# Optimization experiments

Hardware: AMD Instinct MI355X
Metric: run time of the kernel (lower is better)

Reference implementation:

```python
import jax, jax.numpy as jnp
import numpy as np

ENERGY_PERCENT = 0.8


def setup_inputs() -> dict:
    key = jax.random.key(0)
    B, T, C = 32, 4096, 128
    x = jax.random.normal(key, (B, T, C), dtype=jnp.float32)
    return {"x": x}


def reference(x):
    # x: [B, T, C]; FFT along time axis.
    T = x.shape[1]
    xf = jnp.fft.rfft(x, axis=1)                      # [B, F, C] complex
    energies = jnp.abs(xf) ** 2                       # [B, F, C]

    # Sort energies descending along freq axis (per batch, per channel).
    sorted_indices = jnp.argsort(-energies, axis=1)   # [B, F, C] int
    sorted_energies = jnp.take_along_axis(energies, sorted_indices, axis=1)

    total_energy = jnp.sum(energies, axis=1, keepdims=True)        # [B, 1, C]
    cumulative = jnp.cumsum(sorted_energies, axis=1)               # [B, F, C]

    # Smallest k such that cumulative energy exceeds energy_percent of total.
    exceeded = cumulative > total_energy * ENERGY_PERCENT          # [B, F, C] bool
    k = jnp.argmax(exceeded, axis=1) + 1                           # [B, C]

    # rank[b, f, c] = position of frequency f in the descending energy order;
    # this is the inverse permutation of sorted_indices (argsort of a permutation).
    rank = jnp.argsort(sorted_indices, axis=1)                     # [B, F, C]

    is_low_freq = rank < k[:, None, :]                             # [B, F, C]

    # Zero out the high-energy ("low-frequency") components -> residual x_var.
    mask = jnp.where(is_low_freq, 0.0, 1.0).astype(x.dtype)        # [B, F, C]
    x_var = jnp.fft.irfft(xf * mask, n=T, axis=1)                  # [B, T, C]
    x_inv = x - x_var
    return (x_var, x_inv)
```

## Files before the change

### kernel.cpp

```cpp
#include <hip/hip_runtime.h>


#define TLEN 4096
#define N2   2048
#define CCH  128
#define BB   32
#define NSER (BB * CCH)
#define HALF 16777216
#define PI_F 3.14159265358979323846f
#define NT   64
#define TS   64
#define SLAB (CCH * TS)

#define LP(i) ((i) + ((i) >> 5))

__device__ __forceinline__ void cmul(float& r, float& i, float br, float bi) {
  float tr = r * br - i * bi;
  i = r * bi + i * br;
  r = tr;
}

__device__ __forceinline__ void dft4(float vr[4], float vi[4], float s) {
  float t0r = vr[0] + vr[2], t0i = vi[0] + vi[2];
  float t1r = vr[0] - vr[2], t1i = vi[0] - vi[2];
  float t2r = vr[1] + vr[3], t2i = vi[1] + vi[3];
  float d3r = vr[1] - vr[3], d3i = vi[1] - vi[3];
  float t3r = -s * d3i, t3i = s * d3r;
  vr[0] = t0r + t2r; vi[0] = t0i + t2i;
  vr[1] = t1r + t3r; vi[1] = t1i + t3i;
  vr[2] = t0r - t2r; vi[2] = t0i - t2i;
  vr[3] = t1r - t3r; vi[3] = t1i - t3i;
}

__device__ __forceinline__ void dft8(float vr[8], float vi[8], float s) {
  float er[4]  = {vr[0], vr[2], vr[4], vr[6]};
  float ei[4]  = {vi[0], vi[2], vi[4], vi[6]};
  float odr[4] = {vr[1], vr[3], vr[5], vr[7]};
  float odi[4] = {vi[1], vi[3], vi[5], vi[7]};
  dft4(er, ei, s);
  dft4(odr, odi, s);
  const float c = 0.70710678118654752440f;
  float wr[4] = {1.0f, c, 0.0f, -c};
  float wi[4] = {0.0f, s * c, s, s * c};
  #pragma unroll
  for (int k = 0; k < 4; ++k) {
    float tr = wr[k] * odr[k] - wi[k] * odi[k];
    float ti = wr[k] * odi[k] + wi[k] * odr[k];
    vr[k]     = er[k] + tr; vi[k]     = ei[k] + ti;
    vr[k + 4] = er[k] - tr; vi[k + 4] = ei[k] - ti;
  }
}

__device__ __forceinline__ void stage8_first(float* zr, float* zi, int tid, float s) {
  float vr[8], vi[8];
  #pragma unroll
  for (int r = 0; r < 8; ++r) {
    int idx = LP(tid + (r << 8));
    vr[r] = zr[idx]; vi[r] = zi[idx];
  }
  dft8(vr, vi, s);
  __syncthreads();
  #pragma unroll
  for (int r = 0; r < 8; ++r) {
    int idx = LP((tid << 3) + r);
    zr[idx] = vr[r]; zi[idx] = vi[r];
  }
  __syncthreads();
}

template <int NS>
__device__ __forceinline__ void stage8_tw(float* zr, float* zi, int tid, float s) {
  int j = tid;
  int p = j & (NS - 1);
  float vr[8], vi[8];
  #pragma unroll
  for (int r = 0; r < 8; ++r) {
    int idx = LP(j + (r << 8));
    vr[r] = zr[idx]; vi[r] = zi[idx];
  }
  float ang = s * 6.28318530717958647692f * (float)p / (float)(NS * 8);
  float s1, c1; __sincosf(ang, &s1, &c1);
  float c2 = c1 * c1 - s1 * s1, s2 = 2.0f * c1 * s1;
  float c3 = c2 * c1 - s2 * s1, s3 = c2 * s1 + s2 * c1;
  float c4 = c2 * c2 - s2 * s2, s4 = 2.0f * c2 * s2;
  float c5 = c4 * c1 - s4 * s1, s5 = c4 * s1 + s4 * c1;
  float c6 = c4 * c2 - s4 * s2, s6 = c4 * s2 + s4 * c2;
  float c7 = c4 * c3 - s4 * s3, s7 = c4 * s3 + s4 * c3;
  cmul(vr[1], vi[1], c1, s1);
  cmul(vr[2], vi[2], c2, s2);
  cmul(vr[3], vi[3], c3, s3);
  cmul(vr[4], vi[4], c4, s4);
  cmul(vr[5], vi[5], c5, s5);
  cmul(vr[6], vi[6], c6, s6);
  cmul(vr[7], vi[7], c7, s7);
  dft8(vr, vi, s);
  __syncthreads();
  int idxD = ((j - p) << 3) + p;
  #pragma unroll
  for (int r = 0; r < 8; ++r) {
    int idx = LP(idxD + r * NS);
    zr[idx] = vr[r]; zi[idx] = vi[r];
  }
  __syncthreads();
}

__device__ __forceinline__ void stage4_last(float* zr, float* zi, int tid, float s) {
  #pragma unroll
  for (int half = 0; half < 2; ++half) {
    int j = tid + (half << 8);
    float ang = s * PI_F * (float)j * (1.0f / 1024.0f);
    float s1, c1; __sincosf(ang, &s1, &c1);
    float c2 = c1 * c1 - s1 * s1, s2 = 2.0f * c1 * s1;
    float c3 = c2 * c1 - s2 * s1, s3 = c2 * s1 + s2 * c1;
    float vr[4], vi[4];
    #pragma unroll
    for (int r = 0; r < 4; ++r) {
      int idx = LP(j + (r << 9));
      vr[r] = zr[idx]; vi[r] = zi[idx];
    }
    cmul(vr[1], vi[1], c1, s1);
    cmul(vr[2], vi[2], c2, s2);
    cmul(vr[3], vi[3], c3, s3);
    dft4(vr, vi, s);
    #pragma unroll
    for (int r = 0; r < 4; ++r) {
      int idx = LP(j + (r << 9));
      zr[idx] = vr[r]; zi[idx] = vi[r];
    }
  }
  __syncthreads();
}

__device__ __forceinline__ void fft2048(float* zr, float* zi, int tid, float s) {
  stage8_first(zr, zi, tid, s);
  stage8_tw<8>(zr, zi, tid, s);
  stage8_tw<64>(zr, zi, tid, s);
  stage4_last(zr, zi, tid, s);
}

__device__ __forceinline__ float block_sum(float v, float* red, int tid, int bank) {
  #pragma unroll
  for (int o = 32; o > 0; o >>= 1) v += __shfl_down(v, o, 64);
  if ((tid & 63) == 0) red[(bank << 2) + (tid >> 6)] = v;
  __syncthreads();
  int b4 = bank << 2;
  return red[b4] + red[b4 + 1] + red[b4 + 2] + red[b4 + 3];
}

__global__ __launch_bounds__(256) void fourier_filter_series(float* __restrict__ buf) {
  __shared__ float zr[2113], zi[2113];
  __shared__ float red[8];
  int tid = threadIdx.x;
  int b = blockIdx.x >> 7, c = blockIdx.x & 127;
  float* bufp = buf + (size_t)b * (NT * SLAB) + (size_t)c * TS;

  #pragma unroll
  for (int j = 0; j < 8; ++j) {
    int k = tid + (j << 8);
    int off = ((k >> 5) << 13) + ((k & 31) << 1);
    float2 v = *(const float2*)(bufp + off);
    zr[LP(k)] = v.x; zi[LP(k)] = v.y;
  }
  __syncthreads();

  fft2048(zr, zi, tid, -1.0f);

  float eb[9];
  eb[8] = 0.0f;
  const float RC  = 0.92387953251128675613f;
  const float RSn = -0.38268343236508977173f;
  float ws, wc;
  __sincosf(-PI_F * (float)tid * (1.0f / 2048.0f), &ws, &wc);
  #pragma unroll
  for (int jj = 0; jj < 4; ++jj) {
    int k = tid + (jj << 8);
    int mkz = (N2 - k) & (N2 - 1);
    int ik = LP(k), im = LP(N2 - k);
    float akr = zr[ik],      aki = zi[ik];
    float bkr = zr[LP(mkz)], bki = zi[LP(mkz)];
    float Er  = 0.5f * (akr + bkr);
    float Ei  = 0.5f * (aki - bki);
    float Or_ = 0.5f * (aki + bki);
    float Oi  = 0.5f * (bkr - akr);
    float tr = wc * Or_ - ws * Oi;
    float ti = wc * Oi + ws * Or_;
    float x0r = Er + tr, x0i = Ei + ti;
    float x1r = Er - tr, x1i = ti - Ei;
    zr[ik] = x0r; zi[ik] = x0i;
    zr[im] = x1r; zi[im] = x1i;
    eb[2 * jj]     = x0r * x0r + x0i * x0i;
    eb[2 * jj + 1] = x1r * x1r + x1i * x1i;
    float nwc = wc * RC - ws * RSn;
    ws = wc * RSn + ws * RC; wc = nwc;
  }
  if (tid == 0) {
    int i4 = LP(1024);
    float re = zr[i4], im_ = zi[i4];
    zi[i4] = -im_;
    eb[8] = re * re + im_ * im_;
  }

  float tloc = 0.0f;
  #pragma unroll
  for (int s = 0; s < 9; ++s) tloc += eb[s];
  float total = block_sum(tloc, red, tid, 0);
  float thresh = 0.8f * total;

  unsigned lo = 0u, hi = 0x7F7FFFFFu;
  for (int it = 0; it < 31; ++it) {
    unsigned mid = (lo + hi + 1u) >> 1;
    float tau = __uint_as_float(mid);
    float loc = 0.0f;
    #pragma unroll
    for (int s = 0; s < 9; ++s) loc += (eb[s] >= tau) ? eb[s] : 0.0f;
    float ssum = block_sum(loc, red, tid, (it + 1) & 1);
    if (ssum > thresh) lo = mid; else hi = mid - 1;
  }
  float tau = __uint_as_float(lo);

  const float RSp = 0.38268343236508977173f;
  __sincosf(PI_F * (float)tid * (1.0f / 2048.0f), &ws, &wc);
  #pragma unroll
  for (int jj = 0; jj < 4; ++jj) {
    int k = tid + (jj << 8);
    int ik = LP(k), im = LP(N2 - k);
    float xkr = zr[ik], xki = zi[ik];
    float xmr = zr[im], xmi = zi[im];
    float ekk = xkr * xkr + xki * xki;
    float emm = xmr * xmr + xmi * xmi;
    if (ekk >= tau) { xkr = 0.0f; xki = 0.0f; }
    if (emm >= tau) { xmr = 0.0f; xmi = 0.0f; }
    float Er = 0.5f * (xkr + xmr);
    float Ei = 0.5f * (xki - xmi);
    float Br = 0.5f * (xkr - xmr);
    float Bi = 0.5f * (xki + xmi);
    float Or_ = wc * Br - ws * Bi;
    float Oi  = wc * Bi + ws * Br;
    zr[ik] = Er - Oi;  zi[ik] = Ei + Or_;
    zr[im] = Er + Oi;  zi[im] = Or_ - Ei;
    float nwc = wc * RC - ws * RSp;
    ws = wc * RSp + ws * RC; wc = nwc;
  }
  if (tid == 0) {
    int i4 = LP(1024);
    float re = zr[i4], im_ = zi[i4];
    float e = re * re + im_ * im_;
    if (e >= tau) { re = 0.0f; im_ = 0.0f; }
    zr[i4] = re; zi[i4] = -im_;
  }
  __syncthreads();

  fft2048(zr, zi, tid, 1.0f);

  const float scale = 1.0f / 2048.0f;
  #pragma unroll
  for (int j = 0; j < 8; ++j) {
    int k = tid + (j << 8);
    int off = ((k >> 5) << 13) + ((k & 31) << 1);
    float2 v;
    v.x = zr[LP(k)] * scale;
    v.y = zi[LP(k)] * scale;
    *(float2*)(bufp + off) = v;
  }
}

__global__ __launch_bounds__(512) void transpose_fwd(const float* __restrict__ x, float* __restrict__ buf) {
  __shared__ float lds[CCH * 65];
  int tb = blockIdx.x, b = blockIdx.y;
  const float* xp = x + ((size_t)b * TLEN + (size_t)tb * TS) * CCH;
  #pragma unroll
  for (int it = 0; it < 4; ++it) {
    int idx = threadIdx.x + (it << 9);
    int r = idx >> 5, c4 = (idx & 31) << 2;
    float4 v = *(const float4*)(xp + (size_t)r * CCH + c4);
    lds[(c4 + 0) * 65 + r] = v.x;
    lds[(c4 + 1) * 65 + r] = v.y;
    lds[(c4 + 2) * 65 + r] = v.z;
    lds[(c4 + 3) * 65 + r] = v.w;
  }
  __syncthreads();
  float* op = buf + ((size_t)b * NT + tb) * SLAB;
  #pragma unroll
  for (int it = 0; it < 4; ++it) {
    int idx = threadIdx.x + (it << 9);
    int c = idx >> 4, s4 = (idx & 15) << 2;
    float4 v;
    v.x = lds[c * 65 + s4 + 0];
    v.y = lds[c * 65 + s4 + 1];
    v.z = lds[c * 65 + s4 + 2];
    v.w = lds[c * 65 + s4 + 3];
    *(float4*)(op + c * TS + s4) = v;
  }
}

__global__ __launch_bounds__(512) void finalize_t(const float* __restrict__ buf, const float* __restrict__ x,
                                                  float* __restrict__ xvar, float* __restrict__ xinv) {
  __shared__ float lds[TS * 132];
  int tb = blockIdx.x, b = blockIdx.y;
  const float* ip = buf + ((size_t)b * NT + tb) * SLAB;
  #pragma unroll
  for (int it = 0; it < 4; ++it) {
    int idx = threadIdx.x + (it << 9);
    int c = idx >> 4, s4 = (idx & 15) << 2;
    float4 v = *(const float4*)(ip + c * TS + s4);
    lds[(s4 + 0) * 132 + c] = v.x;
    lds[(s4 + 1) * 132 + c] = v.y;
    lds[(s4 + 2) * 132 + c] = v.z;
    lds[(s4 + 3) * 132 + c] = v.w;
  }
  __syncthreads();
  size_t rowbase = ((size_t)b * TLEN + (size_t)tb * TS) * CCH;
  #pragma unroll
  for (int it = 0; it < 4; ++it) {
    int idx = threadIdx.x + (it << 9);
    int t = idx >> 5, c4 = (idx & 31) << 2;
    float4 v = *(const float4*)(&lds[t * 132 + c4]);
    size_t off = rowbase + (size_t)t * CCH + c4;
    float4 xv = *(const float4*)(x + off);
    *(float4*)(xvar + off) = v;
    *(float4*)(xinv + off) = make_float4(xv.x - v.x, xv.y - v.y, xv.z - v.z, xv.w - v.w);
  }
}

extern "C" void kernel_launch(void* const* d_in, const int* in_sizes, int n_in,
                              void* d_out, int out_size, void* d_ws, size_t ws_size,
                              hipStream_t stream) {
  const float* x = (const float*)d_in[0];
  float* out  = (float*)d_out;
  float* xvar = out;
  float* xinv = out + HALF;

  bool use_ws = ws_size >= (size_t)HALF * sizeof(float);
  float* buf = use_ws ? (float*)d_ws : xinv;

  dim3 tgrid(NT, BB);
  transpose_fwd<<<tgrid, 512, 0, stream>>>(x, buf);
  fourier_filter_series<<<NSER, 256, 0, stream>>>(buf);
  finalize_t<<<tgrid, 512, 0, stream>>>(buf, x, xvar, xinv);
}
```

Before: 301.2 us.

## Fuse forward transpose into FFT kernel with strided channel loads and LDS swizzle

The separate transpose_fwd kernel is removed. The FFT kernel now reads each channel's time series straight from x using strided scalar loads, with a block-to-channel remap meant to spread accesses across channels. The launch bound gains a minimum-occupancy hint, and finalize_t XOR-swizzles its LDS indices to cut bank conflicts. This drops one full read and write pass over the buffer and one kernel launch. The cost is uncoalesced 4-byte loads at a 1 KB stride, which depend on L2 reuse across neighbouring channel blocks.

```diff
diff --git a/kernel.cpp b/kernel.cpp
--- a/kernel.cpp
+++ b/kernel.cpp
@@ -147,19 +147,36 @@
   return red[b4] + red[b4 + 1] + red[b4 + 2] + red[b4 + 3];
 }
 
-__global__ __launch_bounds__(256) void fourier_filter_series(float* __restrict__ buf) {
+__global__ __launch_bounds__(256, 8) void fourier_filter_series(const float* __restrict__ x,
+                                                                float* __restrict__ buf) {
   __shared__ float zr[2113], zi[2113];
   __shared__ float red[8];
   int tid = threadIdx.x;
-  int b = blockIdx.x >> 7, c = blockIdx.x & 127;
-  float* bufp = buf + (size_t)b * (NT * SLAB) + (size_t)c * TS;
-
-  #pragma unroll
-  for (int j = 0; j < 8; ++j) {
-    int k = tid + (j << 8);
-    int off = ((k >> 5) << 13) + ((k & 31) << 1);
-    float2 v = *(const float2*)(bufp + off);
-    zr[LP(k)] = v.x; zi[LP(k)] = v.y;
+
+  int bid = blockIdx.x;
+  int r = bid & 7;
+  int m = bid >> 3;
+  int b = m >> 4;
+  int u = m & 15;
+  int c = (((r + b) & 7) << 4) | u;
+
+  const float* xp = x + ((size_t)b * TLEN) * CCH + c;
+  #pragma unroll
+  for (int jb = 0; jb < 2; ++jb) {
+    float re[4], im[4];
+    #pragma unroll
+    for (int j = 0; j < 4; ++j) {
+      int k = tid + (((jb << 2) + j) << 8);
+      int off = k << 8;
+      re[j] = xp[off];
+      im[j] = xp[off + CCH];
+    }
+    #pragma unroll
+    for (int j = 0; j < 4; ++j) {
+      int k = tid + (((jb << 2) + j) << 8);
+      zr[LP(k)] = re[j];
+      zi[LP(k)] = im[j];
+    }
   }
   __syncthreads();
 
@@ -252,6 +269,7 @@
 
   fft2048(zr, zi, tid, 1.0f);
 
+  float* bufp = buf + (size_t)b * (NT * SLAB) + (size_t)c * TS;
   const float scale = 1.0f / 2048.0f;
   #pragma unroll
   for (int j = 0; j < 8; ++j) {
@@ -264,35 +282,6 @@
   }
 }
 
-__global__ __launch_bounds__(512) void transpose_fwd(const float* __restrict__ x, float* __restrict__ buf) {
-  __shared__ float lds[CCH * 65];
-  int tb = blockIdx.x, b = blockIdx.y;
-  const float* xp = x + ((size_t)b * TLEN + (size_t)tb * TS) * CCH;
-  #pragma unroll
-  for (int it = 0; it < 4; ++it) {
-    int idx = threadIdx.x + (it << 9);
-    int r = idx >> 5, c4 = (idx & 31) << 2;
-    float4 v = *(const float4*)(xp + (size_t)r * CCH + c4);
-    lds[(c4 + 0) * 65 + r] = v.x;
-    lds[(c4 + 1) * 65 + r] = v.y;
-    lds[(c4 + 2) * 65 + r] = v.z;
-    lds[(c4 + 3) * 65 + r] = v.w;
-  }
-  __syncthreads();
-  float* op = buf + ((size_t)b * NT + tb) * SLAB;
-  #pragma unroll
-  for (int it = 0; it < 4; ++it) {
-    int idx = threadIdx.x + (it << 9);
-    int c = idx >> 4, s4 = (idx & 15) << 2;
-    float4 v;
-    v.x = lds[c * 65 + s4 + 0];
-    v.y = lds[c * 65 + s4 + 1];
-    v.z = lds[c * 65 + s4 + 2];
-    v.w = lds[c * 65 + s4 + 3];
-    *(float4*)(op + c * TS + s4) = v;
-  }
-}
-
 __global__ __launch_bounds__(512) void finalize_t(const float* __restrict__ buf, const float* __restrict__ x,
                                                   float* __restrict__ xvar, float* __restrict__ xinv) {
   __shared__ float lds[TS * 132];
@@ -303,10 +292,11 @@
     int idx = threadIdx.x + (it << 9);
     int c = idx >> 4, s4 = (idx & 15) << 2;
     float4 v = *(const float4*)(ip + c * TS + s4);
-    lds[(s4 + 0) * 132 + c] = v.x;
-    lds[(s4 + 1) * 132 + c] = v.y;
-    lds[(s4 + 2) * 132 + c] = v.z;
-    lds[(s4 + 3) * 132 + c] = v.w;
+    int cs = c ^ (s4 & 28);
+    lds[(s4 + 0) * 132 + cs] = v.x;
+    lds[(s4 + 1) * 132 + cs] = v.y;
+    lds[(s4 + 2) * 132 + cs] = v.z;
+    lds[(s4 + 3) * 132 + cs] = v.w;
   }
   __syncthreads();
   size_t rowbase = ((size_t)b * TLEN + (size_t)tb * TS) * CCH;
@@ -314,7 +304,8 @@
   for (int it = 0; it < 4; ++it) {
     int idx = threadIdx.x + (it << 9);
     int t = idx >> 5, c4 = (idx & 31) << 2;
-    float4 v = *(const float4*)(&lds[t * 132 + c4]);
+    int key = ((t >> 2) & 7) << 2;
+    float4 v = *(const float4*)(&lds[t * 132 + (c4 ^ key)]);
     size_t off = rowbase + (size_t)t * CCH + c4;
     float4 xv = *(const float4*)(x + off);
     *(float4*)(xvar + off) = v;
@@ -333,8 +324,7 @@
   bool use_ws = ws_size >= (size_t)HALF * sizeof(float);
   float* buf = use_ws ? (float*)d_ws : xinv;
 
+  fourier_filter_series<<<NSER, 256, 0, stream>>>(x, buf);
   dim3 tgrid(NT, BB);
-  transpose_fwd<<<tgrid, 512, 0, stream>>>(x, buf);
-  fourier_filter_series<<<NSER, 256, 0, stream>>>(buf);
   finalize_t<<<tgrid, 512, 0, stream>>>(buf, x, xvar, xinv);
 }
```

Result: no change. 305.2 us (+1.3%).
